# Kernel optimization log

Measured on AMD Instinct MI355X. Metric: run time of the kernel, lower is better.

The kernel has to match this reference:

```python
import jax, jax.numpy as jnp
import numpy as np

K_PRESERVED = 384   # num_preserved_tokens
NUM_HEADS = 6       # config.num_attention_heads // 2


def setup_inputs() -> dict:
    key = jax.random.key(0)
    ks = jax.random.split(key, 10)
    B, L, D, H = 16, 512, 768, 12
    U = D // 2  # num_units of the router attention
    s = 0.02
    return {
        "hidden_states": jax.random.normal(ks[0], (B, L, D), jnp.float32),
        "self_attention_scores": jax.random.uniform(ks[1], (B, H, L, L), jnp.float32),
        "Wq": jax.random.normal(ks[2], (D, U), jnp.float32) * s,
        "bq": jnp.zeros((U,), jnp.float32),
        "Wk": jax.random.normal(ks[3], (D, U), jnp.float32) * s,
        "bk": jnp.zeros((U,), jnp.float32),
        "Wv": jax.random.normal(ks[4], (D, U), jnp.float32) * s,
        "bv": jnp.zeros((U,), jnp.float32),
        "Wo": jax.random.normal(ks[5], (U, D), jnp.float32) * s,
        "bo": jnp.zeros((D,), jnp.float32),
    }


def _forward(hidden_states, self_attention_scores, Wq, bq, Wk, bk, Wv, bv, Wo, bo):
    B, L, D = hidden_states.shape
    K = K_PRESERVED
    r = L - K  # number of tokens merged away by ToMe
    batch_idx = jnp.arange(B)[:, None]

    class_token = hidden_states[:, :1, :]

    # importance = column sums of head-averaged attention with zeroed diagonal (detached)
    s = jax.lax.stop_gradient(jnp.mean(self_attention_scores, axis=1))  # [B,L,L]
    s = s * (1.0 - jnp.eye(L, dtype=s.dtype))
    importance = jnp.sum(s, axis=1)  # [B,L]
    _, important_idx = jax.lax.top_k(importance, K)  # [B,K]
    important_mask = jnp.zeros((B, L), bool).at[batch_idx, important_idx].set(True)

    # --- ToMe bipartite_soft_matching(hidden_states, r), mode='mean' ---
    metric = jax.lax.stop_gradient(hidden_states)
    metric = metric / jnp.linalg.norm(metric, axis=-1, keepdims=True)
    a, b = metric[:, ::2, :], metric[:, 1::2, :]            # [B,L/2,D] each
    sim = jnp.einsum('bid,bjd->bij', a, b)                   # [B,L/2,L/2]
    node_max = jnp.max(sim, axis=-1)                         # [B,L/2]
    node_idx = jnp.argmax(sim, axis=-1)                      # [B,L/2]
    edge_idx = jnp.argsort(-node_max, axis=-1)               # descending
    src_idx = edge_idx[:, :r]                                # merged src tokens
    unm_idx = edge_idx[:, r:]                                # unmerged src tokens
    dst_idx = jnp.take_along_axis(node_idx, src_idx, axis=1)  # [B,r]

    src_x = hidden_states[:, ::2, :]
    dst_x = hidden_states[:, 1::2, :]                        # [B,L/2,D]
    unm = jnp.take_along_axis(src_x, unm_idx[..., None], axis=1)   # [B,L/2-r,D]
    src_sel = jnp.take_along_axis(src_x, src_idx[..., None], axis=1)  # [B,r,D]
    # scatter_reduce(mean, include_self=True): (dst + sum srcs) / (1 + count)
    sums = dst_x.at[batch_idx, dst_idx].add(src_sel)
    counts = jnp.ones((B, L // 2), dst_x.dtype).at[batch_idx, dst_idx].add(1.0)
    dst_merged = sums / counts[..., None]
    preserved_tokens = jnp.concatenate([unm, dst_merged], axis=1)  # [B,K,D]

    # attention_mask is None -> sentences is the first token
    sentences = hidden_states[:, :1, :]

    # unpreserved tokens: boolean-mask gather, preserving original order
    order = jnp.argsort(important_mask.astype(jnp.int32), axis=1, stable=True)
    unp_idx = order[:, : L - K]                              # [B,L-K]
    unpreserved = hidden_states[batch_idx, unp_idx]          # [B,L-K,D]

    # router multi-head attention: query=sentence, key/value=unpreserved
    U = Wq.shape[1]
    hd = U // NUM_HEADS
    q = (sentences @ Wq + bq).reshape(B, 1, NUM_HEADS, hd)
    k = (unpreserved @ Wk + bk).reshape(B, L - K, NUM_HEADS, hd)
    v = (unpreserved @ Wv + bv).reshape(B, L - K, NUM_HEADS, hd)
    att = jax.nn.softmax(jnp.einsum('bqhd,bkhd->bhqk', q, k) / jnp.sqrt(jnp.asarray(hd, q.dtype)), axis=-1)
    ctx = jnp.einsum('bhqk,bkhd->bqhd', att, v).reshape(B, 1, U)
    new_token = ctx @ Wo + bo                                # [B,1,D]

    final_token = jnp.concatenate([class_token, preserved_tokens, new_token], axis=1)  # [B,K+2,D]
    return final_token


def reference(hidden_states, self_attention_scores, Wq, bq, Wk, bk, Wv, bv, Wo, bo):
    return _forward(hidden_states, self_attention_scores, Wq, bq, Wk, bk, Wv, bv, Wo, bo)
```

## Files before the change

kernel.cpp:

```cpp
#include <hip/hip_runtime.h>
#include <hip/hip_bf16.h>

#define BB 16
#define LL 512
#define DD 768
#define NHEAD 12
#define HALF 256
#define KPRES 384
#define RCNT 128
#define UDIM 384
#define NH2 6
#define HD 64

__device__ float              g_colsum_part[BB * NHEAD * 4 * LL];
__device__ unsigned long long g_nodep_part[BB * HALF * 4];
__device__ int                g_unm[BB * RCNT];
__device__ int                g_srctok[BB * RCNT];
__device__ int                g_srcdst[BB * RCNT];
__device__ int                g_unp[BB * RCNT];
__device__ float              g_ctx[BB * UDIM];

__global__ void k_colsum(const float* __restrict__ sc) {
    int blk = blockIdx.x;
    int ic = blk & 3;
    int bh = blk >> 2;
    int j4 = threadIdx.x;
    const float* base = sc + (size_t)bh * LL * LL;
    int i0 = ic * 128;
    float ax = 0.f, ay = 0.f, az = 0.f, aw = 0.f;
    for (int i = 0; i < 128; i++) {
        float4 v = ((const float4*)(base + (size_t)(i0 + i) * LL))[j4];
        ax += v.x; ay += v.y; az += v.z; aw += v.w;
    }
#pragma unroll
    for (int c = 0; c < 4; c++) {
        int cj = 4 * j4 + c;
        if (cj >= i0 && cj < i0 + 128) {
            float d = base[(size_t)cj * LL + cj];
            if (c == 0) ax -= d; else if (c == 1) ay -= d;
            else if (c == 2) az -= d; else aw -= d;
        }
    }
    float* o = &g_colsum_part[(size_t)blk * LL + 4 * j4];
    o[0] = ax; o[1] = ay; o[2] = az; o[3] = aw;
}

__global__ void k_metric(const float* __restrict__ hs, float* __restrict__ metric) {
    int row = blockIdx.x;
    int t = threadIdx.x;
    __shared__ float red[256];
    const float* src = hs + (size_t)row * DD;
    float v0 = src[t], v1 = src[t + 256], v2 = src[t + 512];
    red[t] = ((0.f + v0 * v0) + v1 * v1) + v2 * v2;
    __syncthreads();
    for (int s = 128; s > 0; s >>= 1) {
        if (t < s) red[t] += red[t + s];
        __syncthreads();
    }
    float nrm = sqrtf(red[0]);
    float* dst = metric + (size_t)row * DD;
    dst[t] = v0 / nrm; dst[t + 256] = v1 / nrm; dst[t + 512] = v2 / nrm;
}

__global__ void k_sim(const float* __restrict__ metric) {
    int b = blockIdx.x, it = blockIdx.y, jt = blockIdx.z;
    int i0 = it * 64, j0 = jt * 64;
    __shared__ float As[64][20];
    __shared__ float Bs[64][20];
    __shared__ unsigned long long cand[64][16];
    int t  = threadIdx.x;
    int ti = t >> 4, tj = t & 15;
    float acc[4][4];
#pragma unroll
    for (int a = 0; a < 4; a++)
#pragma unroll
        for (int c = 0; c < 4; c++) acc[a][c] = 0.f;
    const float* mb = metric + (size_t)b * LL * DD;
    int sr = t >> 2, sc4 = t & 3;
    for (int d0 = 0; d0 < DD; d0 += 16) {
        float4 a4 = ((const float4*)(mb + (size_t)(2 * (i0 + sr)) * DD + d0))[sc4];
        float4 b4 = ((const float4*)(mb + (size_t)(2 * (j0 + sr) + 1) * DD + d0))[sc4];
        __syncthreads();
        *(float4*)&As[sr][4 * sc4] = a4;
        *(float4*)&Bs[sr][4 * sc4] = b4;
        __syncthreads();
#pragma unroll
        for (int c4 = 0; c4 < 4; c4++) {
            float av[4][4], bv[4][4];
#pragma unroll
            for (int a = 0; a < 4; a++) {
                float4 v = *(const float4*)&As[ti * 4 + a][4 * c4];
                av[a][0] = v.x; av[a][1] = v.y; av[a][2] = v.z; av[a][3] = v.w;
            }
#pragma unroll
            for (int a = 0; a < 4; a++) {
                float4 v = *(const float4*)&Bs[tj * 4 + a][4 * c4];
                bv[a][0] = v.x; bv[a][1] = v.y; bv[a][2] = v.z; bv[a][3] = v.w;
            }
#pragma unroll
            for (int k = 0; k < 4; k++)
#pragma unroll
                for (int a = 0; a < 4; a++)
#pragma unroll
                    for (int cc = 0; cc < 4; cc++)
                        acc[a][cc] += av[a][k] * bv[cc][k];
        }
    }
#pragma unroll
    for (int a = 0; a < 4; a++) {
        unsigned long long bp = 0ULL;
#pragma unroll
        for (int c = 0; c < 4; c++) {
            int jg = j0 + tj * 4 + c;
            unsigned u = __float_as_uint(acc[a][c]);
            u = (u & 0x80000000u) ? ~u : (u | 0x80000000u);
            unsigned long long p = ((unsigned long long)u << 32) | (unsigned long long)(255 - jg);
            if (p > bp) bp = p;
        }
        cand[ti * 4 + a][tj] = bp;
    }
    __syncthreads();
    if (t < 64) {
        unsigned long long m = cand[t][0];
#pragma unroll
        for (int c2 = 1; c2 < 16; c2++) { unsigned long long v = cand[t][c2]; if (v > m) m = v; }
        g_nodep_part[((size_t)b * HALF + i0 + t) * 4 + jt] = m;
    }
}

__global__ void k_select(int* dummy) {
    int b = blockIdx.x, j = threadIdx.x;
    __shared__ float v[LL];
    __shared__ int pos[LL];
    float imp = 0.f;
    for (int p = 0; p < NHEAD * 4; p++)
        imp += g_colsum_part[((size_t)b * NHEAD * 4 + p) * LL + j];
    v[j] = imp;
    __syncthreads();
    int cnt = 0;
    for (int k = 0; k < LL; k++) {
        float vk = v[k];
        cnt += (vk > imp) || (vk == imp && k < j);
    }
    int notp = (cnt >= KPRES) ? 1 : 0;
    pos[j] = notp;
    __syncthreads();
    for (int s = 1; s < LL; s <<= 1) {
        int add = (j >= s) ? pos[j - s] : 0;
        __syncthreads();
        pos[j] += add;
        __syncthreads();
    }
    if (notp) g_unp[b * RCNT + pos[j] - 1] = j;
}

__global__ void k_edges(int* dummy) {
    int b = blockIdx.x, i = threadIdx.x;
    __shared__ float nm[HALF];
    __shared__ int   ni[HALF];
    unsigned long long p = g_nodep_part[((size_t)b * HALF + i) * 4 + 0];
#pragma unroll
    for (int q = 1; q < 4; q++) {
        unsigned long long w = g_nodep_part[((size_t)b * HALF + i) * 4 + q];
        if (w > p) p = w;
    }
    unsigned u = (unsigned)(p >> 32);
    unsigned bits = (u & 0x80000000u) ? (u & 0x7FFFFFFFu) : ~u;
    float v = __uint_as_float(bits);
    int j = 255 - (int)(p & 0xFFFFFFFFu);
    nm[i] = v; ni[i] = j;
    __syncthreads();
    int cnt = 0;
    for (int k = 0; k < HALF; k++) {
        float vk = nm[k];
        cnt += (vk > v) || (vk == v && k < i);
    }
    if (cnt < RCNT) {
        g_srctok[b * RCNT + cnt] = i;
        g_srcdst[b * RCNT + cnt] = ni[i];
    } else {
        g_unm[b * RCNT + (cnt - RCNT)] = 2 * i;
    }
}

__global__ void k_rows(const float* __restrict__ hs, float* __restrict__ out) {
    int blk = blockIdx.x;
    int row = blk % 385, b = blk / 385;
    int t = threadIdx.x;
    float4* o4 = (float4*)(out + ((size_t)b * 386 + row) * DD);
    if (row == 0) {
        const float4* s4 = (const float4*)(hs + (size_t)b * LL * DD);
        o4[t] = s4[t];
    } else if (row <= RCNT) {
        int tok = g_unm[b * RCNT + row - 1];
        const float4* s4 = (const float4*)(hs + ((size_t)b * LL + tok) * DD);
        o4[t] = s4[t];
    } else {
        int j = row - 1 - RCNT;
        __shared__ int ss[RCNT], sd[RCNT];
        if (t < RCNT) { ss[t] = g_srctok[b * RCNT + t]; sd[t] = g_srcdst[b * RCNT + t]; }
        __syncthreads();
        float4 acc = ((const float4*)(hs + ((size_t)b * LL + 2 * j + 1) * DD))[t];
        float cnt = 1.f;
        for (int s2 = 0; s2 < RCNT; s2++) {
            if (sd[s2] == j) {
                float4 v = ((const float4*)(hs + ((size_t)b * LL + 2 * ss[s2]) * DD))[t];
                acc.x += v.x; acc.y += v.y; acc.z += v.z; acc.w += v.w;
                cnt += 1.f;
            }
        }
        float inv_applied; (void)inv_applied;
        float4 r; r.x = acc.x / cnt; r.y = acc.y / cnt; r.z = acc.z / cnt; r.w = acc.w / cnt;
        o4[t] = r;
    }
}

__global__ void k_attn(const float* __restrict__ hs,
                       const float* __restrict__ Wq, const float* __restrict__ bq,
                       const float* __restrict__ Wk, const float* __restrict__ bk,
                       const float* __restrict__ Wv, const float* __restrict__ bv) {
    int h = blockIdx.x % NH2, b = blockIdx.x / NH2;
    int t = threadIdx.x;
    __shared__ float h0[DD];
    __shared__ float wk2[DD];
    __shared__ float hbar[DD];
    __shared__ float qs[HD];
    __shared__ float red[256];
    __shared__ float att[RCNT];
    __shared__ int   toks[RCNT];
    __shared__ float qbk;
    const float* hb = hs + (size_t)b * LL * DD;
    for (int d = t; d < DD; d += 256) h0[d] = hb[d];
    if (t < RCNT) toks[t] = g_unp[b * RCNT + t];
    __syncthreads();
    {
        int u = t & 63, part = t >> 6;
        float a = 0.f;
        for (int d = part * 192; d < part * 192 + 192; d++)
            a += h0[d] * Wq[(size_t)d * UDIM + h * HD + u];
        red[t] = a;
        __syncthreads();
        if (t < HD)
            qs[t] = bq[h * HD + t] + red[t] + red[t + 64] + red[t + 128] + red[t + 192];
        __syncthreads();
    }
    for (int d = t; d < DD; d += 256) {
        const float4* wrow = (const float4*)(Wk + (size_t)d * UDIM + h * HD);
        const float4* q4 = (const float4*)qs;
        float4 s4 = {0.f, 0.f, 0.f, 0.f};
#pragma unroll
        for (int u4 = 0; u4 < 16; u4++) {
            float4 w = wrow[u4], q = q4[u4];
            s4.x += q.x * w.x; s4.y += q.y * w.y; s4.z += q.z * w.z; s4.w += q.w * w.w;
        }
        wk2[d] = (s4.x + s4.y) + (s4.z + s4.w);
    }
    if (t == 0) {
        float a = 0.f;
        for (int u = 0; u < HD; u++) a += qs[u] * bk[h * HD + u];
        qbk = a;
    }
    __syncthreads();
    float lg = -1e30f;
    if (t < RCNT) {
        const float4* hr4 = (const float4*)(hb + (size_t)toks[t] * DD);
        const float4* wk4 = (const float4*)wk2;
        float4 s4 = {0.f, 0.f, 0.f, 0.f};
        for (int d4 = 0; d4 < DD / 4; d4++) {
            float4 w = wk4[d4], x = hr4[d4];
            s4.x += w.x * x.x; s4.y += w.y * x.y; s4.z += w.z * x.z; s4.w += w.w * x.w;
        }
        lg = (qbk + (s4.x + s4.y) + (s4.z + s4.w)) * 0.125f;
    }
    red[t] = lg;
    __syncthreads();
    for (int s = 128; s > 0; s >>= 1) {
        if (t < s) red[t] = fmaxf(red[t], red[t + s]);
        __syncthreads();
    }
    float mx = red[0];
    __syncthreads();
    float e = (t < RCNT) ? expf(lg - mx) : 0.f;
    red[t] = e;
    __syncthreads();
    for (int s = 128; s > 0; s >>= 1) {
        if (t < s) red[t] += red[t + s];
        __syncthreads();
    }
    float inv = 1.f / red[0];
    __syncthreads();
    if (t < RCNT) att[t] = e * inv;
    __syncthreads();
    if (t < DD / 4) {
        float4 a4 = {0.f, 0.f, 0.f, 0.f};
        for (int s2 = 0; s2 < RCNT; s2++) {
            float w = att[s2];
            float4 x = ((const float4*)(hb + (size_t)toks[s2] * DD))[t];
            a4.x += w * x.x; a4.y += w * x.y; a4.z += w * x.z; a4.w += w * x.w;
        }
        *(float4*)&hbar[4 * t] = a4;
    }
    __syncthreads();
    {
        int u = t & 63, part = t >> 6;
        float a = 0.f;
        for (int d = part * 192; d < part * 192 + 192; d++)
            a += hbar[d] * Wv[(size_t)d * UDIM + h * HD + u];
        red[t] = a;
        __syncthreads();
        if (t < HD)
            g_ctx[b * UDIM + h * HD + t] =
                bv[h * HD + t] + red[t] + red[t + 64] + red[t + 128] + red[t + 192];
    }
}

__global__ void k_newtok(const float* __restrict__ Wo, const float* __restrict__ bo,
                         float* __restrict__ out) {
    int b = blockIdx.x, dd = threadIdx.x;
    __shared__ float c[UDIM];
    if (dd < UDIM) c[dd] = g_ctx[b * UDIM + dd];
    __syncthreads();
    float acc = bo[dd];
    for (int u = 0; u < UDIM; u++)
        acc += c[u] * Wo[(size_t)u * DD + dd];
    out[((size_t)b * 386 + 385) * DD + dd] = acc;
}

extern "C" void kernel_launch(void* const* d_in, const int* in_sizes, int n_in,
                              void* d_out, int out_size, void* d_ws, size_t ws_size,
                              hipStream_t stream) {
    const float* hs = (const float*)d_in[0];
    const float* sc = (const float*)d_in[1];
    const float* Wq = (const float*)d_in[2];
    const float* bq = (const float*)d_in[3];
    const float* Wk = (const float*)d_in[4];
    const float* bk = (const float*)d_in[5];
    const float* Wv = (const float*)d_in[6];
    const float* bv = (const float*)d_in[7];
    const float* Wo = (const float*)d_in[8];
    const float* bo = (const float*)d_in[9];
    float* out = (float*)d_out;
    float* metric = (float*)d_ws;

    k_colsum<<<BB * NHEAD * 4, 128, 0, stream>>>(sc);
    k_metric<<<BB * LL, 256, 0, stream>>>(hs, metric);
    k_sim<<<dim3(BB, 4, 4), 256, 0, stream>>>(metric);
    k_select<<<BB, 512, 0, stream>>>(nullptr);
    k_edges<<<BB, 256, 0, stream>>>(nullptr);
    k_rows<<<BB * 385, 192, 0, stream>>>(hs, out);
    k_attn<<<BB * NH2, 256, 0, stream>>>(hs, Wq, bq, Wk, bk, Wv, bv);
    k_newtok<<<BB, DD, 0, stream>>>(Wo, bo, out);
}
```

Measured before the change: 541.8 us.

## Fuse select/edge kernels, merge newtok into rows, prefetch and transpose sim tiles

```diff
diff --git a/kernel.cpp b/kernel.cpp
--- a/kernel.cpp
+++ b/kernel.cpp
@@ -66,7 +66,7 @@
     int b = blockIdx.x, it = blockIdx.y, jt = blockIdx.z;
     int i0 = it * 64, j0 = jt * 64;
     __shared__ float As[64][20];
-    __shared__ float Bs[64][20];
+    __shared__ float BsT[16][68];
     __shared__ unsigned long long cand[64][16];
     int t  = threadIdx.x;
     int ti = t >> 4, tj = t & 15;
@@ -77,33 +77,40 @@
         for (int c = 0; c < 4; c++) acc[a][c] = 0.f;
     const float* mb = metric + (size_t)b * LL * DD;
     int sr = t >> 2, sc4 = t & 3;
-    for (int d0 = 0; d0 < DD; d0 += 16) {
-        float4 a4 = ((const float4*)(mb + (size_t)(2 * (i0 + sr)) * DD + d0))[sc4];
-        float4 b4 = ((const float4*)(mb + (size_t)(2 * (j0 + sr) + 1) * DD + d0))[sc4];
+    const float* arow = mb + (size_t)(2 * (i0 + sr)) * DD;
+    const float* brow = mb + (size_t)(2 * (j0 + sr) + 1) * DD;
+    float4 a4 = ((const float4*)arow)[sc4];
+    float4 b4 = ((const float4*)brow)[sc4];
+    for (int s = 0; s < 48; s++) {
         __syncthreads();
         *(float4*)&As[sr][4 * sc4] = a4;
-        *(float4*)&Bs[sr][4 * sc4] = b4;
-        __syncthreads();
+        BsT[4 * sc4 + 0][sr] = b4.x;
+        BsT[4 * sc4 + 1][sr] = b4.y;
+        BsT[4 * sc4 + 2][sr] = b4.z;
+        BsT[4 * sc4 + 3][sr] = b4.w;
+        __syncthreads();
+        if (s + 1 < 48) {
+            int d0 = (s + 1) * 16;
+            a4 = ((const float4*)(arow + d0))[sc4];
+            b4 = ((const float4*)(brow + d0))[sc4];
+        }
 #pragma unroll
         for (int c4 = 0; c4 < 4; c4++) {
-            float av[4][4], bv[4][4];
-#pragma unroll
-            for (int a = 0; a < 4; a++) {
-                float4 v = *(const float4*)&As[ti * 4 + a][4 * c4];
-                av[a][0] = v.x; av[a][1] = v.y; av[a][2] = v.z; av[a][3] = v.w;
+            float4 av[4], bk4[4];
+#pragma unroll
+            for (int a = 0; a < 4; a++) av[a] = *(const float4*)&As[ti * 4 + a][4 * c4];
+#pragma unroll
+            for (int k = 0; k < 4; k++) bk4[k] = *(const float4*)&BsT[4 * c4 + k][4 * tj];
+#pragma unroll
+            for (int k = 0; k < 4; k++) {
+#pragma unroll
+                for (int a = 0; a < 4; a++) {
+                    float ak = ((const float*)&av[a])[k];
+#pragma unroll
+                    for (int c = 0; c < 4; c++)
+                        acc[a][c] += ak * ((const float*)&bk4[k])[c];
+                }
             }
-#pragma unroll
-            for (int a = 0; a < 4; a++) {
-                float4 v = *(const float4*)&Bs[tj * 4 + a][4 * c4];
-                bv[a][0] = v.x; bv[a][1] = v.y; bv[a][2] = v.z; bv[a][3] = v.w;
-            }
-#pragma unroll
-            for (int k = 0; k < 4; k++)
-#pragma unroll
-                for (int a = 0; a < 4; a++)
-#pragma unroll
-                    for (int cc = 0; cc < 4; cc++)
-                        acc[a][cc] += av[a][k] * bv[cc][k];
         }
     }
 #pragma unroll
@@ -128,90 +135,58 @@
     }
 }
 
-__global__ void k_select(int* dummy) {
-    int b = blockIdx.x, j = threadIdx.x;
+__global__ void k_seledge(int* dummy) {
+    int b = blockIdx.x, t = threadIdx.x;
     __shared__ float v[LL];
     __shared__ int pos[LL];
+    __shared__ float nm[HALF];
+    __shared__ int   ni[HALF];
     float imp = 0.f;
     for (int p = 0; p < NHEAD * 4; p++)
-        imp += g_colsum_part[((size_t)b * NHEAD * 4 + p) * LL + j];
-    v[j] = imp;
+        imp += g_colsum_part[((size_t)b * NHEAD * 4 + p) * LL + t];
+    v[t] = imp;
     __syncthreads();
     int cnt = 0;
     for (int k = 0; k < LL; k++) {
         float vk = v[k];
-        cnt += (vk > imp) || (vk == imp && k < j);
+        cnt += (vk > imp) || (vk == imp && k < t);
     }
     int notp = (cnt >= KPRES) ? 1 : 0;
-    pos[j] = notp;
+    pos[t] = notp;
     __syncthreads();
     for (int s = 1; s < LL; s <<= 1) {
-        int add = (j >= s) ? pos[j - s] : 0;
-        __syncthreads();
-        pos[j] += add;
-        __syncthreads();
-    }
-    if (notp) g_unp[b * RCNT + pos[j] - 1] = j;
-}
-
-__global__ void k_edges(int* dummy) {
-    int b = blockIdx.x, i = threadIdx.x;
-    __shared__ float nm[HALF];
-    __shared__ int   ni[HALF];
-    unsigned long long p = g_nodep_part[((size_t)b * HALF + i) * 4 + 0];
-#pragma unroll
-    for (int q = 1; q < 4; q++) {
-        unsigned long long w = g_nodep_part[((size_t)b * HALF + i) * 4 + q];
-        if (w > p) p = w;
-    }
-    unsigned u = (unsigned)(p >> 32);
-    unsigned bits = (u & 0x80000000u) ? (u & 0x7FFFFFFFu) : ~u;
-    float v = __uint_as_float(bits);
-    int j = 255 - (int)(p & 0xFFFFFFFFu);
-    nm[i] = v; ni[i] = j;
-    __syncthreads();
-    int cnt = 0;
-    for (int k = 0; k < HALF; k++) {
-        float vk = nm[k];
-        cnt += (vk > v) || (vk == v && k < i);
-    }
-    if (cnt < RCNT) {
-        g_srctok[b * RCNT + cnt] = i;
-        g_srcdst[b * RCNT + cnt] = ni[i];
-    } else {
-        g_unm[b * RCNT + (cnt - RCNT)] = 2 * i;
-    }
-}
-
-__global__ void k_rows(const float* __restrict__ hs, float* __restrict__ out) {
-    int blk = blockIdx.x;
-    int row = blk % 385, b = blk / 385;
-    int t = threadIdx.x;
-    float4* o4 = (float4*)(out + ((size_t)b * 386 + row) * DD);
-    if (row == 0) {
-        const float4* s4 = (const float4*)(hs + (size_t)b * LL * DD);
-        o4[t] = s4[t];
-    } else if (row <= RCNT) {
-        int tok = g_unm[b * RCNT + row - 1];
-        const float4* s4 = (const float4*)(hs + ((size_t)b * LL + tok) * DD);
-        o4[t] = s4[t];
-    } else {
-        int j = row - 1 - RCNT;
-        __shared__ int ss[RCNT], sd[RCNT];
-        if (t < RCNT) { ss[t] = g_srctok[b * RCNT + t]; sd[t] = g_srcdst[b * RCNT + t]; }
-        __syncthreads();
-        float4 acc = ((const float4*)(hs + ((size_t)b * LL + 2 * j + 1) * DD))[t];
-        float cnt = 1.f;
-        for (int s2 = 0; s2 < RCNT; s2++) {
-            if (sd[s2] == j) {
-                float4 v = ((const float4*)(hs + ((size_t)b * LL + 2 * ss[s2]) * DD))[t];
-                acc.x += v.x; acc.y += v.y; acc.z += v.z; acc.w += v.w;
-                cnt += 1.f;
-            }
-        }
-        float inv_applied; (void)inv_applied;
-        float4 r; r.x = acc.x / cnt; r.y = acc.y / cnt; r.z = acc.z / cnt; r.w = acc.w / cnt;
-        o4[t] = r;
+        int add = (t >= s) ? pos[t - s] : 0;
+        __syncthreads();
+        pos[t] += add;
+        __syncthreads();
+    }
+    if (notp) g_unp[b * RCNT + pos[t] - 1] = t;
+    if (t < HALF) {
+        unsigned long long p = g_nodep_part[((size_t)b * HALF + t) * 4 + 0];
+#pragma unroll
+        for (int q = 1; q < 4; q++) {
+            unsigned long long w = g_nodep_part[((size_t)b * HALF + t) * 4 + q];
+            if (w > p) p = w;
+        }
+        unsigned u = (unsigned)(p >> 32);
+        unsigned bits = (u & 0x80000000u) ? (u & 0x7FFFFFFFu) : ~u;
+        nm[t] = __uint_as_float(bits);
+        ni[t] = 255 - (int)(p & 0xFFFFFFFFu);
+    }
+    __syncthreads();
+    if (t < HALF) {
+        float vv = nm[t];
+        int cnt2 = 0;
+        for (int k = 0; k < HALF; k++) {
+            float vk = nm[k];
+            cnt2 += (vk > vv) || (vk == vv && k < t);
+        }
+        if (cnt2 < RCNT) {
+            g_srctok[b * RCNT + cnt2] = t;
+            g_srcdst[b * RCNT + cnt2] = ni[t];
+        } else {
+            g_unm[b * RCNT + (cnt2 - RCNT)] = 2 * t;
+        }
     }
 }
 
@@ -261,17 +236,21 @@
         qbk = a;
     }
     __syncthreads();
-    float lg = -1e30f;
-    if (t < RCNT) {
-        const float4* hr4 = (const float4*)(hb + (size_t)toks[t] * DD);
-        const float4* wk4 = (const float4*)wk2;
+    {
+        int tok = t >> 1, half = t & 1;
+        const float4* hr4 = (const float4*)(hb + (size_t)toks[tok] * DD) + half * 96;
+        const float4* wk4 = (const float4*)wk2 + half * 96;
         float4 s4 = {0.f, 0.f, 0.f, 0.f};
-        for (int d4 = 0; d4 < DD / 4; d4++) {
+        for (int d4 = 0; d4 < 96; d4++) {
             float4 w = wk4[d4], x = hr4[d4];
             s4.x += w.x * x.x; s4.y += w.y * x.y; s4.z += w.z * x.z; s4.w += w.w * x.w;
         }
-        lg = (qbk + (s4.x + s4.y) + (s4.z + s4.w)) * 0.125f;
-    }
+        red[t] = (s4.x + s4.y) + (s4.z + s4.w);
+    }
+    __syncthreads();
+    float lg = -1e30f;
+    if (t < RCNT) lg = (qbk + red[2 * t] + red[2 * t + 1]) * 0.125f;
+    __syncthreads();
     red[t] = lg;
     __syncthreads();
     for (int s = 128; s > 0; s >>= 1) {
@@ -314,16 +293,53 @@
     }
 }
 
-__global__ void k_newtok(const float* __restrict__ Wo, const float* __restrict__ bo,
-                         float* __restrict__ out) {
-    int b = blockIdx.x, dd = threadIdx.x;
-    __shared__ float c[UDIM];
-    if (dd < UDIM) c[dd] = g_ctx[b * UDIM + dd];
-    __syncthreads();
-    float acc = bo[dd];
-    for (int u = 0; u < UDIM; u++)
-        acc += c[u] * Wo[(size_t)u * DD + dd];
-    out[((size_t)b * 386 + 385) * DD + dd] = acc;
+__global__ void k_rows(const float* __restrict__ hs,
+                       const float* __restrict__ Wo, const float* __restrict__ bo,
+                       float* __restrict__ out) {
+    int blk = blockIdx.x;
+    int t = threadIdx.x;
+    if (blk < BB * 385) {
+        int row = blk % 385, b = blk / 385;
+        float4* o4 = (float4*)(out + ((size_t)b * 386 + row) * DD);
+        if (row == 0) {
+            const float4* s4 = (const float4*)(hs + (size_t)b * LL * DD);
+            o4[t] = s4[t];
+        } else if (row <= RCNT) {
+            int tok = g_unm[b * RCNT + row - 1];
+            const float4* s4 = (const float4*)(hs + ((size_t)b * LL + tok) * DD);
+            o4[t] = s4[t];
+        } else {
+            int j = row - 1 - RCNT;
+            __shared__ int ss[RCNT], sd[RCNT];
+            if (t < RCNT) { ss[t] = g_srctok[b * RCNT + t]; sd[t] = g_srcdst[b * RCNT + t]; }
+            __syncthreads();
+            float4 acc = ((const float4*)(hs + ((size_t)b * LL + 2 * j + 1) * DD))[t];
+            float cnt = 1.f;
+            for (int s2 = 0; s2 < RCNT; s2++) {
+                if (sd[s2] == j) {
+                    float4 v = ((const float4*)(hs + ((size_t)b * LL + 2 * ss[s2]) * DD))[t];
+                    acc.x += v.x; acc.y += v.y; acc.z += v.z; acc.w += v.w;
+                    cnt += 1.f;
+                }
+            }
+            float4 r; r.x = acc.x / cnt; r.y = acc.y / cnt; r.z = acc.z / cnt; r.w = acc.w / cnt;
+            o4[t] = r;
+        }
+    } else {
+        int b = blk - BB * 385;
+        __shared__ float c[UDIM];
+        c[t] = g_ctx[b * UDIM + t];
+        c[t + 192] = g_ctx[b * UDIM + t + 192];
+        __syncthreads();
+#pragma unroll
+        for (int kk = 0; kk < 4; kk++) {
+            int dd = t + 192 * kk;
+            float acc = bo[dd];
+            for (int u = 0; u < UDIM; u++)
+                acc += c[u] * Wo[(size_t)u * DD + dd];
+            out[((size_t)b * 386 + 385) * DD + dd] = acc;
+        }
+    }
 }
 
 extern "C" void kernel_launch(void* const* d_in, const int* in_sizes, int n_in,
@@ -345,9 +361,7 @@
     k_colsum<<<BB * NHEAD * 4, 128, 0, stream>>>(sc);
     k_metric<<<BB * LL, 256, 0, stream>>>(hs, metric);
     k_sim<<<dim3(BB, 4, 4), 256, 0, stream>>>(metric);
-    k_select<<<BB, 512, 0, stream>>>(nullptr);
-    k_edges<<<BB, 256, 0, stream>>>(nullptr);
-    k_rows<<<BB * 385, 192, 0, stream>>>(hs, out);
+    k_seledge<<<BB, 512, 0, stream>>>(nullptr);
     k_attn<<<BB * NH2, 256, 0, stream>>>(hs, Wq, bq, Wk, bk, Wv, bv);
-    k_newtok<<<BB, DD, 0, stream>>>(Wo, bo, out);
-}
+    k_rows<<<BB * 385 + BB, 192, 0, stream>>>(hs, Wo, bo, out);
+}
```

After: 527.9 us. 2.6% less time.
